# Performance work log

Hardware: AMD Instinct MI355X
Metric: run time of the kernel (lower is better)

The kernel has to match this reference:

```python
import jax, jax.numpy as jnp
import numpy as np

D_MODEL = 1024
HEADS = 16
D_K = D_MODEL // HEADS
THETA = 10000.0


def _rope(x, pos):
    # x: [B, H, S, d_k]; pos: [S]
    half = D_K // 2
    inv_freq = 1.0 / (THETA ** (jnp.arange(0, D_K, 2, dtype=jnp.float32) / D_K))  # [half]
    ang = pos.astype(jnp.float32)[:, None] * inv_freq[None, :]  # [S, half]
    cos, sin = jnp.cos(ang), jnp.sin(ang)
    x1 = x[..., 0::2]  # even components
    x2 = x[..., 1::2]  # odd components
    o1 = x1 * cos - x2 * sin
    o2 = x1 * sin + x2 * cos
    # interleave back to original layout
    out = jnp.stack([o1, o2], axis=-1).reshape(x.shape)
    return out


def setup_inputs() -> dict:
    key = jax.random.key(0)
    ks = jax.random.split(key, 5)
    B, S = 4, 2048
    scale = 1.0 / np.sqrt(D_MODEL)
    return {
        "x": jax.random.normal(ks[0], (B, S, D_MODEL), dtype=jnp.float32),
        "Wq": jax.random.normal(ks[1], (D_MODEL, D_MODEL), dtype=jnp.float32) * scale,
        "Wk": jax.random.normal(ks[2], (D_MODEL, D_MODEL), dtype=jnp.float32) * scale,
        "Wv": jax.random.normal(ks[3], (D_MODEL, D_MODEL), dtype=jnp.float32) * scale,
        "Wo": jax.random.normal(ks[4], (D_MODEL, D_MODEL), dtype=jnp.float32) * scale,
    }


def reference(x, Wq, Wk, Wv, Wo):
    B, S, _ = x.shape
    # Linear weights are [out, in]; y = x @ W.T
    def proj(W):
        y = jnp.einsum('bsd,ed->bse', x, W)
        return y.reshape(B, S, HEADS, D_K).transpose(0, 2, 1, 3)  # [B,H,S,d_k]
    Q, K, V = proj(Wq), proj(Wk), proj(Wv)
    pos = jnp.arange(S, dtype=jnp.int32)
    Q = _rope(Q, pos)
    K = _rope(K, pos)
    scores = jnp.einsum('bhqd,bhkd->bhqk', Q, K) / jnp.sqrt(jnp.float32(D_K))
    causal = jnp.tril(jnp.ones((S, S), dtype=bool))
    scores = jnp.where(causal, scores, jnp.finfo(scores.dtype).min)
    attn = jax.nn.softmax(scores, axis=-1)
    mh = jnp.einsum('bhqk,bhkd->bhqd', attn, V)  # [B,H,S,d_v]
    mh = mh.transpose(0, 2, 1, 3).reshape(B, S, D_MODEL)
    return jnp.einsum('bsd,ed->bse', mh, Wo)
```

## Files before the change

kernel.cpp:

```cpp
#include <hip/hip_runtime.h>

typedef unsigned short u16;
typedef unsigned int   u32;
typedef __attribute__((ext_vector_type(8))) short s16x8;
typedef __attribute__((ext_vector_type(4))) float f32x4;
typedef __attribute__((ext_vector_type(16))) float f32x16;
typedef __attribute__((ext_vector_type(2))) int i32x2;

#define D_MODEL 1024
#define S_LEN   2048
#define BATCH   4
#define HEADS   16
#define DK      64
#define M_TOTAL (BATCH * S_LEN)

#define QSCALE 0.18033688011112042f
#define ROPE_L2 0.41524101186092029f

__device__ __forceinline__ u16 f2b(float f) {
  u32 u = __float_as_uint(f);
  u32 r = u + 0x7FFFu + ((u >> 16) & 1u);
  return (u16)(r >> 16);
}
__device__ __forceinline__ u32 packtrunc(float f0, float f1) {
  return (__float_as_uint(f0) >> 16) | (__float_as_uint(f1) & 0xFFFF0000u);
}
__device__ __forceinline__ u32 packrn(float f0, float f1) {
  return (u32)f2b(f0) | ((u32)f2b(f1) << 16);
}

extern "C" __device__ float __ocml_native_exp2_f32(float);
__device__ __forceinline__ float fexp2(float x) {
#if __has_builtin(__builtin_amdgcn_exp2f)
  return __builtin_amdgcn_exp2f(x);
#else
  return __ocml_native_exp2_f32(x);
#endif
}

template<int N> __device__ __forceinline__ void waitvm() {
  asm volatile("s_waitcnt vmcnt(%0)" :: "n"(N) : "memory");
}
template<int N> __device__ __forceinline__ void waitlgkm() {
  asm volatile("s_waitcnt lgkmcnt(%0)" :: "n"(N) : "memory");
}

template<int OFF> __device__ __forceinline__ s16x8 ldsr(unsigned a) {
  s16x8 r;
  asm volatile("ds_read_b128 %0, %1 offset:%2" : "=v"(r) : "v"(a), "n"(OFF));
  return r;
}

typedef const __attribute__((address_space(1))) unsigned int* gas_u32p;
typedef __attribute__((address_space(3))) unsigned int* las_u32p;
#define GLL16(gp, lp) __builtin_amdgcn_global_load_lds((gas_u32p)(gp), (las_u32p)(lp), 16, 0, 0)

__global__ void k_cvt(const float* __restrict__ x,
                      const float* __restrict__ a, const float* __restrict__ b,
                      const float* __restrict__ c, const float* __restrict__ d,
                      u16* __restrict__ Xb, u16* __restrict__ Wb) {
  int i = blockIdx.x * blockDim.x + threadIdx.x;
  if (i < 2097152) {
    float4 v = ((const float4*)x)[i];
    ((u32*)Xb)[2 * i]     = packrn(v.x, v.y);
    ((u32*)Xb)[2 * i + 1] = packrn(v.z, v.w);
  } else {
    int j = i - 2097152;
    const float* src = (j < 524288) ? ((j < 262144) ? a : b) : ((j < 786432) ? c : d);
    float4 v = ((const float4*)src)[j & 0x3FFFF];
    ((u32*)Wb)[2 * j]     = packrn(v.x, v.y);
    ((u32*)Wb)[2 * j + 1] = packrn(v.z, v.w);
  }
}

template<int GX, bool BF16OUT, bool ROPE, bool DUAL>
__launch_bounds__(256, 3)
__global__ void k_gemm3(const u16* __restrict__ A, const u16* __restrict__ B,
                        void* __restrict__ C, void* __restrict__ C2,
                        int N, int K, float scale) {
  constexpr int SLOT = 8192;
  __shared__ u16 SH[3 * SLOT];
  const int tid  = threadIdx.x;
  const int lane = tid & 63;
  const int w    = tid >> 6;
  const int wm2  = w >> 1, wn2 = w & 1;
  const int rl   = lane & 15, q = lane >> 4;

  const int nwg = gridDim.x;
  const int bid = (blockIdx.x & 7) * (nwg >> 3) + (blockIdx.x >> 3);
  const int bx = bid % GX, by = bid / GX;
  const int bm = by * 128, bn = bx * 128;

  const int rowS = tid >> 2;
  const int blkS = (tid & 3) ^ ((lane >> 3) & 3);
  const u16* Asrc = A + (size_t)(bm + rowS) * K + blkS * 8;
  const u16* Bsrc = B + (size_t)(bn + rowS) * K + blkS * 8;

  const unsigned shb = (unsigned)(size_t)(las_u32p)SH;
  const int fbase = rl * 32 + ((q ^ ((rl >> 1) & 3)) * 8);
  unsigned aR = shb + 2 * (wm2 * 2048 + fbase);
  unsigned bR = shb + 2 * (4096 + wn2 * 2048 + fbase);

  f32x4 acc[4][4];
#pragma unroll
  for (int i = 0; i < 4; i++)
#pragma unroll
    for (int j = 0; j < 4; j++) acc[i][j] = (f32x4){0.f, 0.f, 0.f, 0.f};

  const int nt = K >> 5;

  auto stage = [&](int t, int eoff) {
    const int k0 = t << 5;
    u16* d = SH + eoff + w * 512;
#pragma unroll
    for (int s2 = 0; s2 < 2; s2++) {
      GLL16(Asrc + (size_t)(s2 * 64) * K + k0, d + s2 * 2048);
      GLL16(Bsrc + (size_t)(s2 * 64) * K + k0, d + 4096 + s2 * 2048);
    }
  };

  stage(0, 0);
  stage(1, SLOT);
  int pslot = 2 * SLOT;

  for (int t = 0; t < nt; t++) {
    if (t < nt - 1) waitvm<4>();
    else            waitvm<0>();
    __builtin_amdgcn_s_barrier();

    s16x8 bf0 = ldsr<0>(bR),    bf1 = ldsr<1024>(bR);
    s16x8 bf2 = ldsr<2048>(bR), bf3 = ldsr<3072>(bR);
    s16x8 af0 = ldsr<0>(aR),    af1 = ldsr<1024>(aR);
    s16x8 af2 = ldsr<2048>(aR), af3 = ldsr<3072>(aR);

    if (t + 2 < nt) stage(t + 2, pslot);

    waitlgkm<3>();
    __builtin_amdgcn_sched_barrier(0);
    __builtin_amdgcn_s_setprio(1);
    acc[0][0] = __builtin_amdgcn_mfma_f32_16x16x32_bf16(af0, bf0, acc[0][0], 0, 0, 0);
    acc[0][1] = __builtin_amdgcn_mfma_f32_16x16x32_bf16(af0, bf1, acc[0][1], 0, 0, 0);
    acc[0][2] = __builtin_amdgcn_mfma_f32_16x16x32_bf16(af0, bf2, acc[0][2], 0, 0, 0);
    acc[0][3] = __builtin_amdgcn_mfma_f32_16x16x32_bf16(af0, bf3, acc[0][3], 0, 0, 0);
    waitlgkm<2>();
    __builtin_amdgcn_sched_barrier(0);
    acc[1][0] = __builtin_amdgcn_mfma_f32_16x16x32_bf16(af1, bf0, acc[1][0], 0, 0, 0);
    acc[1][1] = __builtin_amdgcn_mfma_f32_16x16x32_bf16(af1, bf1, acc[1][1], 0, 0, 0);
    acc[1][2] = __builtin_amdgcn_mfma_f32_16x16x32_bf16(af1, bf2, acc[1][2], 0, 0, 0);
    acc[1][3] = __builtin_amdgcn_mfma_f32_16x16x32_bf16(af1, bf3, acc[1][3], 0, 0, 0);
    waitlgkm<1>();
    __builtin_amdgcn_sched_barrier(0);
    acc[2][0] = __builtin_amdgcn_mfma_f32_16x16x32_bf16(af2, bf0, acc[2][0], 0, 0, 0);
    acc[2][1] = __builtin_amdgcn_mfma_f32_16x16x32_bf16(af2, bf1, acc[2][1], 0, 0, 0);
    acc[2][2] = __builtin_amdgcn_mfma_f32_16x16x32_bf16(af2, bf2, acc[2][2], 0, 0, 0);
    acc[2][3] = __builtin_amdgcn_mfma_f32_16x16x32_bf16(af2, bf3, acc[2][3], 0, 0, 0);
    waitlgkm<0>();
    __builtin_amdgcn_sched_barrier(0);
    acc[3][0] = __builtin_amdgcn_mfma_f32_16x16x32_bf16(af3, bf0, acc[3][0], 0, 0, 0);
    acc[3][1] = __builtin_amdgcn_mfma_f32_16x16x32_bf16(af3, bf1, acc[3][1], 0, 0, 0);
    acc[3][2] = __builtin_amdgcn_mfma_f32_16x16x32_bf16(af3, bf2, acc[3][2], 0, 0, 0);
    acc[3][3] = __builtin_amdgcn_mfma_f32_16x16x32_bf16(af3, bf3, acc[3][3], 0, 0, 0);
    __builtin_amdgcn_s_setprio(0);

    aR = (aR >= shb + 2 * 2 * SLOT) ? aR - 2 * 2 * SLOT : aR + 2 * SLOT;
    bR = (bR >= shb + 2 * 2 * SLOT + 8192) ? bR - 2 * 2 * SLOT : bR + 2 * SLOT;
    pslot = (pslot == 2 * SLOT) ? 0 : pslot + SLOT;
  }

  const bool isQ = !DUAL || (bn < D_MODEL);
  u16* Cd = (u16*)(isQ ? C : C2);
  const int bnL = DUAL ? (bn & (D_MODEL - 1)) : bn;
  const float sc = isQ ? scale : 1.0f;

#pragma unroll
  for (int mi = 0; mi < 4; mi++)
#pragma unroll
    for (int ni = 0; ni < 4; ni++) {
      if (ROPE) {
        const int col = bnL + wn2 * 64 + ni * 16 + rl;
        const int fi  = (col & 63) >> 1;
        const float inv = exp2f(-(float)fi * ROPE_L2);
        const bool odd = (rl & 1);
#pragma unroll
        for (int r = 0; r < 4; r++) {
          int grow = bm + wm2 * 64 + mi * 16 + q * 4 + r;
          float own = acc[mi][ni][r];
          float oth = __shfl_xor(own, 1);
          float ang = (float)(grow & (S_LEN - 1)) * inv;
          float sn, cs;
          __sincosf(ang, &sn, &cs);
          float x1 = odd ? oth : own;
          float x2 = odd ? own : oth;
          float res = odd ? (x1 * sn + x2 * cs) : (x1 * cs - x2 * sn);
          acc[mi][ni][r] = res * sc;
        }
      }
#pragma unroll
      for (int r = 0; r < 4; r++) {
        int grow = bm + wm2 * 64 + mi * 16 + q * 4 + r;
        int gcol = bnL + wn2 * 64 + ni * 16 + rl;
        float v = acc[mi][ni][r];
        if (BF16OUT) Cd[(size_t)grow * N + gcol] = f2b(v);
        else         ((float*)Cd)[(size_t)grow * N + gcol] = v;
      }
    }
}

__launch_bounds__(256, 4)
__global__ void k_attn(const u16* __restrict__ Qb, const u16* __restrict__ Kb,
                       const u16* __restrict__ Vtg, u16* __restrict__ Mh) {
  __shared__ u16 SH[128 * 64 + 64 * 128];
  u16* Kl = SH;
  u16* Vt = SH + 128 * 64;
  const int tid  = threadIdx.x;
  const int lane = tid & 63;
  const int w    = tid >> 6;
  const int n    = lane & 31;
  const int h    = lane >> 5;
  const int nx   = n & 7;
  const int bid = blockIdx.x;
  const int r   = bid >> 3;
  const int u   = r & 15;
  const int bh  = (bid & 7) + 8 * (r >> 4);
  const int hd  = bh & 15, b = bh >> 4;
  const int s   = (w & 2) ? (62 - 2 * u + (w & 1)) : (2 * u + (w & 1));
  const int rb  = s * 32;
  const int ktiles = ((63 - 2 * u) >> 2) + 1;
  const size_t kbase = ((size_t)b * S_LEN) * D_MODEL + (size_t)hd * DK;
  const size_t vbase = ((size_t)hd * DK) * M_TOTAL + (size_t)b * S_LEN;

  const int hx    = ((h ^ nx) << 3);
  const int kidx0 = n * 64  + hx;
  const int vidx0 = n * 128 + hx;

  s16x8 bq[4];
#pragma unroll
  for (int ks = 0; ks < 4; ks++)
    bq[ks] = *(const s16x8*)(Qb + kbase + (size_t)(rb + n) * D_MODEL + ks * 16 + h * 8);

  f32x16 o[2];
#pragma unroll
  for (int dt = 0; dt < 2; dt++)
#pragma unroll
    for (int i = 0; i < 16; i++) o[dt][i] = 0.f;
  float psum = 0.f;

  const int krow_l = lane >> 3;
  const int kblk_l = (lane & 7) ^ krow_l;
  const u16* KgL = Kb + kbase + (size_t)(w * 32 + krow_l) * D_MODEL + kblk_l * 8;
  u16* KdL = Kl + (w * 32) * 64;
  const int vrow_l = lane >> 4;
  const int vblk_l = lane & 15;
  const u16* VgL = Vtg + vbase + (size_t)(w * 16 + vrow_l) * M_TOTAL;
  u16* VdL = Vt + (w * 16) * 128;

  for (int t = 0; t < ktiles; t++) {
    const int k0 = t * 128;
    __syncthreads();
#pragma unroll
    for (int i = 0; i < 4; i++)
      GLL16(KgL + (size_t)(k0 + i * 8) * D_MODEL, KdL + i * 8 * 64);
#pragma unroll
    for (int i = 0; i < 4; i++) {
      const int jj = vblk_l ^ ((i * 4 + vrow_l) & 7);
      GLL16(VgL + (size_t)(i * 4) * M_TOTAL + k0 + jj * 8, VdL + i * 4 * 128);
    }
    __syncthreads();

#pragma unroll
    for (int kt = 0; kt < 4; kt++) {
      const int k0t = k0 + kt * 32;
      if (k0t > rb + 31) continue;

      s16x8 ak[4], vf[4];
#pragma unroll
      for (int ks = 0; ks < 4; ks++)
        ak[ks] = *(const s16x8*)(Kl + ((kidx0 ^ (ks << 4)) + kt * 2048));
#pragma unroll
      for (int c = 0; c < 2; c++)
#pragma unroll
        for (int dt = 0; dt < 2; dt++)
          vf[c * 2 + dt] = *(const s16x8*)(Vt + ((vidx0 ^ (kt * 32 + c * 16)) + dt * 4096));

      f32x16 Sc;
#pragma unroll
      for (int i = 0; i < 16; i++) Sc[i] = 0.f;
#pragma unroll
      for (int ks = 0; ks < 4; ks++)
        Sc = __builtin_amdgcn_mfma_f32_32x32x16_bf16(ak[ks], bq[ks], Sc, 0, 0, 0);

      u32 P0[4], P1[4];
      float ps01 = 0.f, ps23 = 0.f;
      if ((k0t + 31) > rb) {
        const int lim = rb + n - k0t - 4 * h;
#pragma unroll
        for (int g = 0; g < 4; g++) {
          float pv[4];
#pragma unroll
          for (int t2 = 0; t2 < 4; t2++) {
            float e = fexp2(Sc[4 * g + t2]);
            pv[t2] = (8 * g + t2 <= lim) ? e : 0.f;
          }
          ps01 += pv[0] + pv[1];
          ps23 += pv[2] + pv[3];
          P0[g] = packtrunc(pv[0], pv[1]);
          P1[g] = packtrunc(pv[2], pv[3]);
        }
      } else {
#pragma unroll
        for (int g = 0; g < 4; g++) {
          float pv[4];
#pragma unroll
          for (int t2 = 0; t2 < 4; t2++) pv[t2] = fexp2(Sc[4 * g + t2]);
          ps01 += pv[0] + pv[1];
          ps23 += pv[2] + pv[3];
          P0[g] = packtrunc(pv[0], pv[1]);
          P1[g] = packtrunc(pv[2], pv[3]);
        }
      }
      psum += ps01 + ps23;

#pragma unroll
      for (int c = 0; c < 2; c++) {
        i32x2 rA = __builtin_amdgcn_permlane32_swap((int)P0[2 * c], (int)P0[2 * c + 1], false, false);
        i32x2 rB = __builtin_amdgcn_permlane32_swap((int)P1[2 * c], (int)P1[2 * c + 1], false, false);
        union { u32 uu[4]; s16x8 v; } pb;
        pb.uu[0] = (u32)rA[0];
        pb.uu[1] = (u32)rB[0];
        pb.uu[2] = (u32)rA[1];
        pb.uu[3] = (u32)rB[1];
        o[0] = __builtin_amdgcn_mfma_f32_32x32x16_bf16(vf[c * 2 + 0], pb.v, o[0], 0, 0, 0);
        o[1] = __builtin_amdgcn_mfma_f32_32x32x16_bf16(vf[c * 2 + 1], pb.v, o[1], 0, 0, 0);
      }
    }
  }

  float l = psum + __shfl_xor(psum, 32);
  const float linv = 1.0f / l;
  __syncthreads();
  u16* Olw = SH + w * 32 * 66;
#pragma unroll
  for (int dt = 0; dt < 2; dt++) {
#pragma unroll
    for (int g = 0; g < 4; g++) {
      u32 lo = packrn(o[dt][4 * g + 0] * linv, o[dt][4 * g + 1] * linv);
      u32 hi = packrn(o[dt][4 * g + 2] * linv, o[dt][4 * g + 3] * linv);
      *(uint2*)(Olw + n * 66 + dt * 32 + 8 * g + 4 * h) = (uint2){lo, hi};
    }
  }
  const int rr = lane >> 3, seg = lane & 7;
#pragma unroll
  for (int ro = 0; ro < 32; ro += 8) {
    uint4 v = *(const uint4*)(Olw + (ro + rr) * 66 + seg * 8);
    *(uint4*)(Mh + ((size_t)b * S_LEN + rb + ro + rr) * D_MODEL + hd * DK + seg * 8) = v;
  }
}

extern "C" void kernel_launch(void* const* d_in, const int* in_sizes, int n_in,
                              void* d_out, int out_size, void* d_ws, size_t ws_size,
                              hipStream_t stream) {
  const float* x  = (const float*)d_in[0];
  const float* Wq = (const float*)d_in[1];
  const float* Wk = (const float*)d_in[2];
  const float* Wv = (const float*)d_in[3];
  const float* Wo = (const float*)d_in[4];
  float* out = (float*)d_out;

  char* ws = (char*)d_ws;
  const size_t xsz = (size_t)M_TOTAL * D_MODEL * 2;
  const size_t wsz = (size_t)D_MODEL * D_MODEL * 2;
  u16* Xb  = (u16*)ws; ws += xsz;
  u16* Wqb = (u16*)ws; ws += wsz;
  u16* Wkb = (u16*)ws; ws += wsz;
  u16* Wvb = (u16*)ws; ws += wsz;
  u16* Wob = (u16*)ws; ws += wsz;
  u16* Qb  = (u16*)ws; ws += xsz;
  u16* Kb  = (u16*)ws; ws += xsz;
  u16* Vtg = (u16*)ws; ws += xsz;
  u16* Mh  = (u16*)ws; ws += xsz;

  k_cvt<<<12288, 256, 0, stream>>>(x, Wq, Wk, Wv, Wo, Xb, Wqb);

  k_gemm3<16, true, true, true><<<1024, 256, 0, stream>>>(
      Xb, Wqb, Qb, Kb, D_MODEL, D_MODEL, QSCALE);
  k_gemm3<64, true, false, false><<<512, 256, 0, stream>>>(
      Wvb, Xb, Vtg, Vtg, M_TOTAL, D_MODEL, 1.0f);

  k_attn<<<dim3(1024), 256, 0, stream>>>(Qb, Kb, Vtg, Mh);

  k_gemm3<8, false, false, false><<<512, 256, 0, stream>>>(
      Mh, Wob, out, out, D_MODEL, D_MODEL, 1.0f);
}
```

Measured before the change: 244.6 us.

## Merge QK and V projections into one launch, switch GEMM to double buffering

Fuses the QK-projection GEMM and the transposed V-projection GEMM into a single 1536-block launch that dispatches on a swizzled block index, and gives the output projection its own wrapper. The shared GEMM body goes from a three-slot LDS ring with two tiles in flight to a two-slot double buffer with a full vmcnt(0) wait each iteration. LDS use drops from 48KB to 32KB and launch bounds rise to 4 blocks per CU. The aim is to remove one launch and its tail and to raise occupancy, at the cost of less prefetch depth and more exposed global-load latency per k-step.

```diff
diff --git a/kernel.cpp b/kernel.cpp
--- a/kernel.cpp
+++ b/kernel.cpp
@@ -73,24 +73,18 @@
   }
 }
 
-template<int GX, bool BF16OUT, bool ROPE, bool DUAL>
-__launch_bounds__(256, 3)
-__global__ void k_gemm3(const u16* __restrict__ A, const u16* __restrict__ B,
-                        void* __restrict__ C, void* __restrict__ C2,
-                        int N, int K, float scale) {
+template<bool BF16OUT, bool ROPE, bool DUAL>
+__device__ __forceinline__ void gemm_body(u16* __restrict__ SH,
+                                          const u16* __restrict__ A, const u16* __restrict__ B,
+                                          void* __restrict__ C, void* __restrict__ C2,
+                                          int bm, int bn, int N, int K, float scale) {
   constexpr int SLOT = 8192;
-  __shared__ u16 SH[3 * SLOT];
   const int tid  = threadIdx.x;
   const int lane = tid & 63;
   const int w    = tid >> 6;
   const int wm2  = w >> 1, wn2 = w & 1;
   const int rl   = lane & 15, q = lane >> 4;
 
-  const int nwg = gridDim.x;
-  const int bid = (blockIdx.x & 7) * (nwg >> 3) + (blockIdx.x >> 3);
-  const int bx = bid % GX, by = bid / GX;
-  const int bm = by * 128, bn = bx * 128;
-
   const int rowS = tid >> 2;
   const int blkS = (tid & 3) ^ ((lane >> 3) & 3);
   const u16* Asrc = A + (size_t)(bm + rowS) * K + blkS * 8;
@@ -98,8 +92,8 @@
 
   const unsigned shb = (unsigned)(size_t)(las_u32p)SH;
   const int fbase = rl * 32 + ((q ^ ((rl >> 1) & 3)) * 8);
-  unsigned aR = shb + 2 * (wm2 * 2048 + fbase);
-  unsigned bR = shb + 2 * (4096 + wn2 * 2048 + fbase);
+  const unsigned aR0 = shb + 2 * (wm2 * 2048 + fbase);
+  const unsigned bR0 = shb + 2 * (4096 + wn2 * 2048 + fbase);
 
   f32x4 acc[4][4];
 #pragma unroll
@@ -109,31 +103,29 @@
 
   const int nt = K >> 5;
 
-  auto stage = [&](int t, int eoff) {
+  auto stage = [&](int t) {
     const int k0 = t << 5;
-    u16* d = SH + eoff + w * 512;
-#pragma unroll
-    for (int s2 = 0; s2 < 2; s2++) {
-      GLL16(Asrc + (size_t)(s2 * 64) * K + k0, d + s2 * 2048);
-      GLL16(Bsrc + (size_t)(s2 * 64) * K + k0, d + 4096 + s2 * 2048);
-    }
+    u16* d = SH + (t & 1) * SLOT + w * 512;
+    GLL16(Asrc + k0, d);
+    GLL16(Asrc + (size_t)64 * K + k0, d + 2048);
+    GLL16(Bsrc + k0, d + 4096);
+    GLL16(Bsrc + (size_t)64 * K + k0, d + 6144);
   };
 
-  stage(0, 0);
-  stage(1, SLOT);
-  int pslot = 2 * SLOT;
+  stage(0);
 
   for (int t = 0; t < nt; t++) {
-    if (t < nt - 1) waitvm<4>();
-    else            waitvm<0>();
+    waitvm<0>();
     __builtin_amdgcn_s_barrier();
 
+    const unsigned off = (unsigned)((t & 1) * (2 * SLOT));
+    const unsigned aR = aR0 + off, bR = bR0 + off;
     s16x8 bf0 = ldsr<0>(bR),    bf1 = ldsr<1024>(bR);
     s16x8 bf2 = ldsr<2048>(bR), bf3 = ldsr<3072>(bR);
     s16x8 af0 = ldsr<0>(aR),    af1 = ldsr<1024>(aR);
     s16x8 af2 = ldsr<2048>(aR), af3 = ldsr<3072>(aR);
 
-    if (t + 2 < nt) stage(t + 2, pslot);
+    if (t + 1 < nt) stage(t + 1);
 
     waitlgkm<3>();
     __builtin_amdgcn_sched_barrier(0);
@@ -161,10 +153,6 @@
     acc[3][2] = __builtin_amdgcn_mfma_f32_16x16x32_bf16(af3, bf2, acc[3][2], 0, 0, 0);
     acc[3][3] = __builtin_amdgcn_mfma_f32_16x16x32_bf16(af3, bf3, acc[3][3], 0, 0, 0);
     __builtin_amdgcn_s_setprio(0);
-
-    aR = (aR >= shb + 2 * 2 * SLOT) ? aR - 2 * 2 * SLOT : aR + 2 * SLOT;
-    bR = (bR >= shb + 2 * 2 * SLOT + 8192) ? bR - 2 * 2 * SLOT : bR + 2 * SLOT;
-    pslot = (pslot == 2 * SLOT) ? 0 : pslot + SLOT;
   }
 
   const bool isQ = !DUAL || (bn < D_MODEL);
@@ -204,6 +192,34 @@
         else         ((float*)Cd)[(size_t)grow * N + gcol] = v;
       }
     }
+}
+
+__launch_bounds__(256, 4)
+__global__ void k_qkv(const u16* __restrict__ Xb, const u16* __restrict__ Wqkb,
+                      const u16* __restrict__ Wvb,
+                      u16* __restrict__ Qb, u16* __restrict__ Kb, u16* __restrict__ Vtg) {
+  __shared__ u16 SH[16384];
+  const int swz = (blockIdx.x & 7) * 192 + (blockIdx.x >> 3);
+  if (swz < 1024) {
+    gemm_body<true, true, true>(SH, Xb, Wqkb, Qb, Kb,
+                                (swz >> 4) * 128, (swz & 15) * 128,
+                                D_MODEL, D_MODEL, QSCALE);
+  } else {
+    const int b2 = swz - 1024;
+    gemm_body<true, false, false>(SH, Wvb, Xb, Vtg, Vtg,
+                                  (b2 >> 6) * 128, (b2 & 63) * 128,
+                                  M_TOTAL, D_MODEL, 1.0f);
+  }
+}
+
+__launch_bounds__(256, 4)
+__global__ void k_out(const u16* __restrict__ Mh, const u16* __restrict__ Wob,
+                      float* __restrict__ out) {
+  __shared__ u16 SH[16384];
+  const int swz = (blockIdx.x & 7) * 64 + (blockIdx.x >> 3);
+  gemm_body<false, false, false>(SH, Mh, Wob, out, out,
+                                 (swz >> 3) * 128, (swz & 7) * 128,
+                                 D_MODEL, D_MODEL, 1.0f);
 }
 
 __launch_bounds__(256, 4)
@@ -381,13 +397,9 @@
 
   k_cvt<<<12288, 256, 0, stream>>>(x, Wq, Wk, Wv, Wo, Xb, Wqb);
 
-  k_gemm3<16, true, true, true><<<1024, 256, 0, stream>>>(
-      Xb, Wqb, Qb, Kb, D_MODEL, D_MODEL, QSCALE);
-  k_gemm3<64, true, false, false><<<512, 256, 0, stream>>>(
-      Wvb, Xb, Vtg, Vtg, M_TOTAL, D_MODEL, 1.0f);
+  k_qkv<<<1536, 256, 0, stream>>>(Xb, Wqb, Wvb, Qb, Kb, Vtg);
 
   k_attn<<<dim3(1024), 256, 0, stream>>>(Qb, Kb, Vtg, Mh);
 
-  k_gemm3<8, false, false, false><<<512, 256, 0, stream>>>(
-      Mh, Wob, out, out, D_MODEL, D_MODEL, 1.0f);
-}
+  k_out<<<512, 256, 0, stream>>>(Mh, Wob, out);
+}
```

Result: no change. 245.2 us (+0.2%).
